# Kernel optimization log

Hardware: AMD Instinct MI355X
Metric: run time of the kernel (lower is better)

## Reference

```python
import jax, jax.numpy as jnp
import numpy as np


def setup_inputs() -> dict:
    key = jax.random.key(0)
    k1, k2 = jax.random.split(key)
    B, N, M = 8, 8192, 8192
    source_points = jax.random.normal(k1, (B, N, 3), dtype=jnp.float32)
    target_points = jax.random.normal(k2, (B, M, 3), dtype=jnp.float32)
    return {"source_points": source_points, "target_points": target_points}


def reference(source_points, target_points):
    # dist: [B, N, M]  (same math as (x[:, :, None] - y[:, None]) ** 2 summed over coords)
    s_sq = jnp.sum(source_points ** 2, axis=-1)  # [B, N]
    t_sq = jnp.sum(target_points ** 2, axis=-1)  # [B, M]
    cross = jnp.einsum("bnd,bmd->bnm", source_points, target_points)  # [B, N, M]
    dist = s_sq[:, :, None] + t_sq[:, None, :] - 2.0 * cross
    min_s2t = jnp.min(dist, axis=2)  # [B, N] nearest target for each source point
    min_t2s = jnp.min(dist, axis=1)  # [B, M] nearest source for each target point
    chamfer = jnp.mean(min_s2t, axis=1) + jnp.mean(min_t2s, axis=1)  # [B]
    return chamfer
```

## Files before the change

kernel.cpp:

```cpp
#include <hip/hip_runtime.h>


typedef float f32x16 __attribute__((ext_vector_type(16)));
typedef short bf16x8 __attribute__((ext_vector_type(8)));

constexpr int BATCH  = 8;
constexpr int NPTS   = 8192;
constexpr int BLOCK  = 256;
constexpr int QTILE  = 256;
constexpr int QB     = NPTS / QTILE;
constexpr int DSPLIT = 2;
constexpr int DBR    = NPTS / DSPLIT;
constexpr int CH     = 256;
constexpr int NCH    = DBR / CH;

constexpr size_t FRAG_N = (size_t)BATCH * NPTS * 2;
constexpr size_t SM_N   = (size_t)BATCH * NPTS;

static __device__ __forceinline__ float fmin3(float a, float b, float c) {
    return fminf(fminf(a, b), c);
}
static __device__ __forceinline__ unsigned short bf16h(float f) {
    unsigned int u = __float_as_uint(f);
    u += 0x7fffu + ((u >> 16) & 1u);
    return (unsigned short)(u >> 16);
}
static __device__ __forceinline__ float bf16tof(unsigned short h) {
    return __uint_as_float(((unsigned int)h) << 16);
}
static __device__ __forceinline__ unsigned int pack2(unsigned short a, unsigned short b) {
    return (unsigned int)a | ((unsigned int)b << 16);
}

static __device__ __forceinline__ void make_bfrag(float px, float py, float pz,
                                                  uint4& p0, uint4& p1) {
    const unsigned short one = bf16h(1.0f);
    float nx = -px, ny = -py, nz = -pz;
    float ht = 0.5f * fmaf(px, px, fmaf(py, py, pz * pz));
    unsigned short nxh = bf16h(nx), nxl = bf16h(nx - bf16tof(nxh));
    unsigned short nyh = bf16h(ny), nyl = bf16h(ny - bf16tof(nyh));
    unsigned short nzh = bf16h(nz), nzl = bf16h(nz - bf16tof(nzh));
    unsigned short hh = bf16h(ht),  hl = bf16h(ht - bf16tof(hh));
    p0 = make_uint4(pack2(nxh, nxl), pack2(nxh, nyh),
                    pack2(nyl, nyh), pack2(nzh, nzl));
    p1 = make_uint4(pack2(nzh, one), pack2(one, hh),
                    pack2(hl, 0), 0u);
}

__global__ __launch_bounds__(BLOCK) void chamfer_prep(
    const float* __restrict__ src, const float* __restrict__ tgt,
    uint4* __restrict__ fragS, uint4* __restrict__ fragT,
    unsigned int* __restrict__ mins, float* __restrict__ out)
{
    const int i = blockIdx.x * BLOCK + threadIdx.x;
    uint4 p0, p1;
    const float* tp = tgt + (size_t)i * 3;
    make_bfrag(tp[0], tp[1], tp[2], p0, p1);
    fragT[2 * i + 0] = p0;
    fragT[2 * i + 1] = p1;
    const float* sp = src + (size_t)i * 3;
    make_bfrag(sp[0], sp[1], sp[2], p0, p1);
    fragS[2 * i + 0] = p0;
    fragS[2 * i + 1] = p1;
    mins[i]        = 0x7f7f7f7fu;
    mins[SM_N + i] = 0x7f7f7f7fu;
    if (i < BATCH) out[i] = 0.0f;
}

__global__ __launch_bounds__(BLOCK) void chamfer_nn(
    const float* __restrict__ src, const float* __restrict__ tgt,
    const uint4* __restrict__ fragS, const uint4* __restrict__ fragT,
    unsigned int* __restrict__ mins)
{
    __shared__ uint4 Bfr0[CH], Bfr1[CH];

    const int tid  = threadIdx.x;
    const int lane = tid & 63;
    const int w    = tid >> 6;
    const int half = lane >> 5;
    const int l31  = lane & 31;
    const int qb   = blockIdx.x;
    const int b    = blockIdx.y;
    const int dir  = blockIdx.z / DSPLIT;
    const int ds   = blockIdx.z % DSPLIT;

    const float* P  = dir ? tgt : src;
    const uint4* FB = dir ? fragS : fragT;

    const unsigned short one = bf16h(1.0f);
    bf16x8 af0, af1;
#pragma unroll
    for (int g = 0; g < 2; g++) {
        const int q = qb * QTILE + w * 64 + g * 32 + l31;
        const float* qp = P + ((size_t)b * NPTS + q) * 3;
        float qx = qp[0], qy = qp[1], qz = qp[2];
        float hq = 0.5f * fmaf(qx, qx, fmaf(qy, qy, qz * qz));
        unsigned short xh = bf16h(qx), xl = bf16h(qx - bf16tof(xh));
        unsigned short yh = bf16h(qy), yl = bf16h(qy - bf16tof(yh));
        unsigned short zh = bf16h(qz), zl = bf16h(qz - bf16tof(zh));
        unsigned short qh = bf16h(hq), ql = bf16h(hq - bf16tof(qh));
        bf16x8 a;
        if (half == 0) {
            a[0] = (short)xh; a[1] = (short)xh; a[2] = (short)xl;
            a[3] = (short)yh; a[4] = (short)yh; a[5] = (short)yl;
            a[6] = (short)zh; a[7] = (short)zh;
        } else {
            a[0] = (short)zl; a[1] = (short)qh; a[2] = (short)ql;
            a[3] = (short)one; a[4] = (short)one;
            a[5] = 0; a[6] = 0; a[7] = 0;
        }
        if (g == 0) af0 = a; else af1 = a;
    }

    float rmn0[16], rmn1[16];
#pragma unroll
    for (int r = 0; r < 16; r++) { rmn0[r] = 3.4e38f; rmn1[r] = 3.4e38f; }
    const f32x16 zz = {};
    const uint4* Bh = half ? Bfr1 : Bfr0;

    const uint4* fb = FB + ((size_t)b * NPTS + (size_t)ds * DBR) * 2;

    uint4 r0 = fb[2 * tid + 0], r1 = fb[2 * tid + 1];

    for (int c = 0; c < NCH; ++c) {
        __syncthreads();
        Bfr0[tid] = r0;
        Bfr1[tid] = r1;
        __syncthreads();
        if (c + 1 < NCH) {
            r0 = fb[2 * ((c + 1) * CH + tid) + 0];
            r1 = fb[2 * ((c + 1) * CH + tid) + 1];
        }

#pragma unroll
        for (int tp = 0; tp < CH / 64; ++tp) {
            const int t0 = tp * 2, t1 = tp * 2 + 1;
            bf16x8 b0 = *reinterpret_cast<const bf16x8*>(&Bh[t0 * 32 + l31]);
            bf16x8 b1 = *reinterpret_cast<const bf16x8*>(&Bh[t1 * 32 + l31]);
            f32x16 a00 = __builtin_amdgcn_mfma_f32_32x32x16_bf16(af0, b0, zz, 0, 0, 0);
            f32x16 a01 = __builtin_amdgcn_mfma_f32_32x32x16_bf16(af0, b1, zz, 0, 0, 0);
            f32x16 a10 = __builtin_amdgcn_mfma_f32_32x32x16_bf16(af1, b0, zz, 0, 0, 0);
            f32x16 a11 = __builtin_amdgcn_mfma_f32_32x32x16_bf16(af1, b1, zz, 0, 0, 0);
#pragma unroll
            for (int r = 0; r < 16; r++) {
                rmn0[r] = fmin3(rmn0[r], a00[r], a01[r]);
                rmn1[r] = fmin3(rmn1[r], a10[r], a11[r]);
            }
        }
    }

    unsigned int* M = mins + ((size_t)dir * BATCH + b) * NPTS;
    const int qbase = qb * QTILE + w * 64;
#pragma unroll
    for (int r = 0; r < 16; r++) {
        float a = rmn0[r], bv = rmn1[r];
#pragma unroll
        for (int off = 16; off > 0; off >>= 1) {
            a  = fminf(a,  __shfl_xor(a,  off, 64));
            bv = fminf(bv, __shfl_xor(bv, off, 64));
        }
        if (l31 == 0) {
            const int row = (r & 3) + 8 * (r >> 2) + 4 * half;
            atomicMin(&M[qbase + row],      __float_as_uint(fmaxf(a,  0.0f)));
            atomicMin(&M[qbase + 32 + row], __float_as_uint(fmaxf(bv, 0.0f)));
        }
    }
}

__global__ __launch_bounds__(BLOCK) void chamfer_final(
    const unsigned int* __restrict__ mins, float* __restrict__ out)
{
    const int seg = blockIdx.x;
    const int b   = blockIdx.y;
    const int tid = threadIdx.x;
    float acc = 0.0f;
#pragma unroll
    for (int k = 0; k < 8; k++) {
        const size_t i = (size_t)b * NPTS + seg * 2048 + k * BLOCK + tid;
        acc += __uint_as_float(mins[i]) + __uint_as_float(mins[SM_N + i]);
    }
    for (int off = 32; off > 0; off >>= 1) acc += __shfl_down(acc, off, 64);
    __shared__ float wsum[4];
    if ((tid & 63) == 0) wsum[tid >> 6] = acc;
    __syncthreads();
    if (tid == 0)
        atomicAdd(&out[b],
                  (wsum[0] + wsum[1] + wsum[2] + wsum[3]) * (2.0f / (float)NPTS));
}

extern "C" void kernel_launch(void* const* d_in, const int* in_sizes, int n_in,
                              void* d_out, int out_size, void* d_ws, size_t ws_size,
                              hipStream_t stream) {
    const float* src = (const float*)d_in[0];
    const float* tgt = (const float*)d_in[1];
    float* out = (float*)d_out;

    uint4* fragT        = (uint4*)d_ws;
    uint4* fragS        = fragT + FRAG_N;
    unsigned int* mins  = (unsigned int*)(fragS + FRAG_N);

    chamfer_prep<<<BATCH * NPTS / BLOCK, BLOCK, 0, stream>>>(
        src, tgt, fragS, fragT, mins, out);
    chamfer_nn<<<dim3(QB, BATCH, 2 * DSPLIT), BLOCK, 0, stream>>>(
        src, tgt, fragS, fragT, mins);
    chamfer_final<<<dim3(4, BATCH), BLOCK, 0, stream>>>(mins, out);
}
```

Baseline: 111.8 us.

## Load MFMA B fragments directly from global memory and remap grid for locality

Result: faster. 103.1 us (-7.8%).

```diff
diff --git a/kernel.cpp b/kernel.cpp
--- a/kernel.cpp
+++ b/kernel.cpp
@@ -8,11 +8,12 @@
 constexpr int NPTS   = 8192;
 constexpr int BLOCK  = 256;
 constexpr int QTILE  = 256;
+constexpr int NAF    = 2;
 constexpr int QB     = NPTS / QTILE;
-constexpr int DSPLIT = 2;
+constexpr int DSPLIT = 4;
 constexpr int DBR    = NPTS / DSPLIT;
-constexpr int CH     = 256;
-constexpr int NCH    = DBR / CH;
+constexpr int NT     = DBR / 32;
+constexpr int NBLK   = QB * BATCH * 2 * DSPLIT;
 
 constexpr size_t FRAG_N = (size_t)BATCH * NPTS * 2;
 constexpr size_t SM_N   = (size_t)BATCH * NPTS;
@@ -67,31 +68,34 @@
     if (i < BATCH) out[i] = 0.0f;
 }
 
-__global__ __launch_bounds__(BLOCK) void chamfer_nn(
+__global__ __launch_bounds__(BLOCK, 2) void chamfer_nn(
     const float* __restrict__ src, const float* __restrict__ tgt,
     const uint4* __restrict__ fragS, const uint4* __restrict__ fragT,
     unsigned int* __restrict__ mins)
 {
-    __shared__ uint4 Bfr0[CH], Bfr1[CH];
-
     const int tid  = threadIdx.x;
     const int lane = tid & 63;
     const int w    = tid >> 6;
     const int half = lane >> 5;
     const int l31  = lane & 31;
-    const int qb   = blockIdx.x;
-    const int b    = blockIdx.y;
-    const int dir  = blockIdx.z / DSPLIT;
-    const int ds   = blockIdx.z % DSPLIT;
+
+    const int lin  = blockIdx.x;
+    const int rest = lin >> 3;
+    const int qb   = rest & 31;
+    const int p    = ((rest >> 5) << 3) | (lin & 7);
+    const int b    = p & 7;
+    const int z    = p >> 3;
+    const int dir  = z >> 2;
+    const int ds   = z & 3;
 
     const float* P  = dir ? tgt : src;
     const uint4* FB = dir ? fragS : fragT;
 
     const unsigned short one = bf16h(1.0f);
-    bf16x8 af0, af1;
-#pragma unroll
-    for (int g = 0; g < 2; g++) {
-        const int q = qb * QTILE + w * 64 + g * 32 + l31;
+    bf16x8 af[NAF];
+#pragma unroll
+    for (int g = 0; g < NAF; g++) {
+        const int q = qb * QTILE + w * (32 * NAF) + g * 32 + l31;
         const float* qp = P + ((size_t)b * NPTS + q) * 3;
         float qx = qp[0], qy = qp[1], qz = qp[2];
         float hq = 0.5f * fmaf(qx, qx, fmaf(qy, qy, qz * qz));
@@ -109,48 +113,38 @@
             a[3] = (short)one; a[4] = (short)one;
             a[5] = 0; a[6] = 0; a[7] = 0;
         }
-        if (g == 0) af0 = a; else af1 = a;
+        af[g] = a;
     }
 
     float rmn0[16], rmn1[16];
 #pragma unroll
     for (int r = 0; r < 16; r++) { rmn0[r] = 3.4e38f; rmn1[r] = 3.4e38f; }
     const f32x16 zz = {};
-    const uint4* Bh = half ? Bfr1 : Bfr0;
-
-    const uint4* fb = FB + ((size_t)b * NPTS + (size_t)ds * DBR) * 2;
-
-    uint4 r0 = fb[2 * tid + 0], r1 = fb[2 * tid + 1];
-
-    for (int c = 0; c < NCH; ++c) {
-        __syncthreads();
-        Bfr0[tid] = r0;
-        Bfr1[tid] = r1;
-        __syncthreads();
-        if (c + 1 < NCH) {
-            r0 = fb[2 * ((c + 1) * CH + tid) + 0];
-            r1 = fb[2 * ((c + 1) * CH + tid) + 1];
-        }
-
-#pragma unroll
-        for (int tp = 0; tp < CH / 64; ++tp) {
-            const int t0 = tp * 2, t1 = tp * 2 + 1;
-            bf16x8 b0 = *reinterpret_cast<const bf16x8*>(&Bh[t0 * 32 + l31]);
-            bf16x8 b1 = *reinterpret_cast<const bf16x8*>(&Bh[t1 * 32 + l31]);
-            f32x16 a00 = __builtin_amdgcn_mfma_f32_32x32x16_bf16(af0, b0, zz, 0, 0, 0);
-            f32x16 a01 = __builtin_amdgcn_mfma_f32_32x32x16_bf16(af0, b1, zz, 0, 0, 0);
-            f32x16 a10 = __builtin_amdgcn_mfma_f32_32x32x16_bf16(af1, b0, zz, 0, 0, 0);
-            f32x16 a11 = __builtin_amdgcn_mfma_f32_32x32x16_bf16(af1, b1, zz, 0, 0, 0);
-#pragma unroll
-            for (int r = 0; r < 16; r++) {
-                rmn0[r] = fmin3(rmn0[r], a00[r], a01[r]);
-                rmn1[r] = fmin3(rmn1[r], a10[r], a11[r]);
-            }
+
+    const uint4* gp = FB + ((size_t)b * NPTS + (size_t)ds * DBR) * 2
+                         + 2 * l31 + half;
+
+    uint4 c0 = gp[0], c1 = gp[64];
+    for (int t = 0; t < NT; t += 2) {
+        bf16x8 b0 = __builtin_bit_cast(bf16x8, c0);
+        bf16x8 b1 = __builtin_bit_cast(bf16x8, c1);
+        if (t + 2 < NT) {
+            c0 = gp[64 * (t + 2)];
+            c1 = gp[64 * (t + 3)];
+        }
+        f32x16 a00 = __builtin_amdgcn_mfma_f32_32x32x16_bf16(af[0], b0, zz, 0, 0, 0);
+        f32x16 a01 = __builtin_amdgcn_mfma_f32_32x32x16_bf16(af[0], b1, zz, 0, 0, 0);
+        f32x16 a10 = __builtin_amdgcn_mfma_f32_32x32x16_bf16(af[1], b0, zz, 0, 0, 0);
+        f32x16 a11 = __builtin_amdgcn_mfma_f32_32x32x16_bf16(af[1], b1, zz, 0, 0, 0);
+#pragma unroll
+        for (int r = 0; r < 16; r++) {
+            rmn0[r] = fmin3(rmn0[r], a00[r], a01[r]);
+            rmn1[r] = fmin3(rmn1[r], a10[r], a11[r]);
         }
     }
 
     unsigned int* M = mins + ((size_t)dir * BATCH + b) * NPTS;
-    const int qbase = qb * QTILE + w * 64;
+    const int qbase = qb * QTILE + w * (32 * NAF);
 #pragma unroll
     for (int r = 0; r < 16; r++) {
         float a = rmn0[r], bv = rmn1[r];
@@ -201,7 +195,7 @@
 
     chamfer_prep<<<BATCH * NPTS / BLOCK, BLOCK, 0, stream>>>(
         src, tgt, fragS, fragT, mins, out);
-    chamfer_nn<<<dim3(QB, BATCH, 2 * DSPLIT), BLOCK, 0, stream>>>(
+    chamfer_nn<<<NBLK, BLOCK, 0, stream>>>(
         src, tgt, fragS, fragT, mins);
     chamfer_final<<<dim3(4, BATCH), BLOCK, 0, stream>>>(mins, out);
 }
```
